# Kernel tuning notes

Hardware: AMD Instinct MI355X
Metric: run time of the kernel (lower is better)

The kernel has to match this reference:

```python
import jax, jax.numpy as jnp
import numpy as np

EPS = 1e-5

def layer_norm(x, w, b):
    mu = jnp.mean(x, axis=-1, keepdims=True)
    var = jnp.mean(jnp.square(x - mu), axis=-1, keepdims=True)
    return (x - mu) * jax.lax.rsqrt(var + EPS) * w + b

def setup_inputs() -> dict:
    key = jax.random.key(0)
    ks = jax.random.split(key, 8)
    B, T, C = 8, 512, 768
    s = 1.0 / np.sqrt(C)
    s4 = 1.0 / np.sqrt(4 * C)
    return {
        "x": jax.random.normal(ks[0], (B, T, C), dtype=jnp.float32),
        "ln1_w": jnp.ones((C,), jnp.float32),
        "ln1_b": jnp.zeros((C,), jnp.float32),
        "Wr": jax.random.normal(ks[1], (C, C), dtype=jnp.float32) * s,
        "Wk": jax.random.normal(ks[2], (C, C), dtype=jnp.float32) * s,
        "Wv": jax.random.normal(ks[3], (C, C), dtype=jnp.float32) * s,
        "time_mix_w": jnp.ones((C,), jnp.float32),  # torch init: torch.ones(n_embd)
        "Wrouter": jax.random.normal(ks[4], (C, C), dtype=jnp.float32) * s,
        "ln2_w": jnp.ones((C,), jnp.float32),
        "ln2_b": jnp.zeros((C,), jnp.float32),
        "Wck": jax.random.normal(ks[5], (4 * C, C), dtype=jnp.float32) * s,
        "Wcv": jax.random.normal(ks[6], (C, 4 * C), dtype=jnp.float32) * s4,
    }

def reference(x, ln1_w, ln1_b, Wr, Wk, Wv, time_mix_w, Wrouter, ln2_w, ln2_b, Wck, Wcv):
    B, T, C = x.shape
    xx = layer_norm(x, ln1_w, ln1_b)
    r = xx @ Wr.T
    k = xx @ Wk.T
    v = xx @ Wv.T
    w = -jnp.exp(time_mix_w)                        # (C,) negative per-channel decay rate
    idx = jnp.arange(T)
    diff = jnp.clip(idx[:, None] - idx[None, :], 0).astype(x.dtype)  # (T,T) t-j clamped at 0
    causal = jnp.tril(jnp.ones((T, T), x.dtype))
    decay = jnp.exp(w[:, None, None] * diff[None]) * causal          # (C,T,T)
    kv = k * v                                                       # (B,T,C)
    # wkv[b,t,c] = sum_j decay[c,t,j] * kv[b,j,c]
    wkv = jnp.einsum('ctj,bjc->btc', decay, kv)
    routed_wkv = wkv * jax.nn.sigmoid(xx @ Wrouter.T)
    x = x + r * routed_wkv
    xx2 = layer_norm(x, ln2_w, ln2_b)
    k_cm = jnp.square(jax.nn.relu(xx2 @ Wck.T))                      # (B,T,4C)
    return x + k_cm @ Wcv.T
```

## Files before the change

### kernel.cpp

```cpp
#include <hip/hip_runtime.h>
#include <hip/hip_bf16.h>

typedef __bf16 bf16_t;
typedef __bf16 bf16x8 __attribute__((ext_vector_type(8)));
typedef __bf16 bf16x4 __attribute__((ext_vector_type(4)));
typedef float  f32x4  __attribute__((ext_vector_type(4)));

#define LN_EPS 1e-5f


typedef __attribute__((address_space(1))) void gvoid_t;
typedef __attribute__((address_space(3))) void lvoid_t;
__device__ __forceinline__ void glds16(const void* g, void* l) {
    __builtin_amdgcn_global_load_lds((gvoid_t*)g, (lvoid_t*)l, 16, 0, 0);
}

__global__ __launch_bounds__(256) void k_cvt4(const float* __restrict__ s0,
                                              const float* __restrict__ s1,
                                              const float* __restrict__ s2,
                                              const float* __restrict__ s3,
                                              bf16_t* __restrict__ dst, int n4) {
    const float* s = (blockIdx.y == 0) ? s0 : (blockIdx.y == 1) ? s1 : (blockIdx.y == 2) ? s2 : s3;
    bf16_t* d = dst + (size_t)blockIdx.y * ((size_t)n4 * 4);
    int i = blockIdx.x * 256 + threadIdx.x;
    if (i < n4) {
        float4 v = ((const float4*)s)[i];
        bf16x4 o;
        o.x = (bf16_t)v.x; o.y = (bf16_t)v.y; o.z = (bf16_t)v.z; o.w = (bf16_t)v.w;
        ((bf16x4*)d)[i] = o;
    }
}

__global__ __launch_bounds__(256) void k_cvt2(const float* __restrict__ s0,
                                              const float* __restrict__ s1,
                                              bf16_t* __restrict__ dst, int n4) {
    const float* s = (blockIdx.y == 0) ? s0 : s1;
    bf16_t* d = dst + (size_t)blockIdx.y * ((size_t)n4 * 4);
    int i = blockIdx.x * 256 + threadIdx.x;
    if (i < n4) {
        float4 v = ((const float4*)s)[i];
        bf16x4 o;
        o.x = (bf16_t)v.x; o.y = (bf16_t)v.y; o.z = (bf16_t)v.z; o.w = (bf16_t)v.w;
        ((bf16x4*)d)[i] = o;
    }
}

__global__ __launch_bounds__(256) void k_ln(const float* __restrict__ x,
                                            const float* __restrict__ w,
                                            const float* __restrict__ b,
                                            bf16_t* __restrict__ out, int C) {
    int row = blockIdx.x;
    const float* xr = x + (long)row * C;
    int tid = threadIdx.x;
    float s = 0.f, s2 = 0.f;
    for (int i = tid; i < C; i += 256) { float v = xr[i]; s += v; s2 += v * v; }
    for (int m = 32; m; m >>= 1) { s += __shfl_xor(s, m, 64); s2 += __shfl_xor(s2, m, 64); }
    __shared__ float red[8];
    int wv = tid >> 6;
    if ((tid & 63) == 0) { red[wv] = s; red[4 + wv] = s2; }
    __syncthreads();
    float ts  = red[0] + red[1] + red[2] + red[3];
    float ts2 = red[4] + red[5] + red[6] + red[7];
    float mu  = ts / C;
    float var = ts2 / C - mu * mu;
    float rstd = rsqrtf(var + LN_EPS);
    bf16_t* orow = out + (long)row * C;
    for (int i = tid; i < C; i += 256)
        orow[i] = (bf16_t)((xr[i] - mu) * rstd * w[i] + b[i]);
}

template <int EPI>
__global__ __launch_bounds__(256) void k_gemm_bt(const bf16_t* __restrict__ A,
                                                 const bf16_t* __restrict__ Bw,
                                                 void* __restrict__ Cout,
                                                 int N, int Ktot, int nbn, int nks) {
    constexpr int TBUF = 128 * 32;
    __shared__ __align__(16) bf16_t As[3][128][32];
    __shared__ __align__(16) bf16_t Bs[3][128][32];
    const int tid  = threadIdx.x;
    const int lane = tid & 63, wid = tid >> 6;
    const int wm = (wid >> 1) * 64, wn = (wid & 1) * 64;

    int nwg = gridDim.x;
    int cpx = nwg >> 3;
    int bid = blockIdx.x;
    int swz = (bid & 7) * cpx + (bid >> 3);
    int per_m = nbn * nks;
    int bm  = swz / per_m;
    int rem = swz % per_m;
    int ks  = rem / nbn;
    int bn  = rem % nbn;

    const int fr = lane & 15;
    const int swcol = ((lane >> 4) ^ (fr & 3)) * 8;

    f32x4 acc[4][4];
#pragma unroll
    for (int i = 0; i < 4; i++)
#pragma unroll
        for (int j = 0; j < 4; j++) acc[i][j] = (f32x4){0.f, 0.f, 0.f, 0.f};

    const int srow = wid * 16 + (lane >> 2);
    const int scol = ((lane & 3) ^ ((lane >> 2) & 3)) * 8;
    const bf16_t* Ag = A  + (size_t)(bm * 128 + srow) * Ktot + (size_t)ks * 768 + scol;
    const bf16_t* Bg = Bw + (size_t)(bn * 128 + srow) * Ktot + (size_t)ks * 768 + scol;
    const size_t rowK64 = (size_t)64 * Ktot;
    bf16_t* lA = &As[0][wid * 16][0];
    bf16_t* lB = &Bs[0][wid * 16][0];

#define STAGE(buf, kt)                                              \
    do {                                                            \
        glds16(Ag + (kt),          lA + (buf) * TBUF);              \
        glds16(Ag + (kt) + rowK64, lA + (buf) * TBUF + 64 * 32);    \
        glds16(Bg + (kt),          lB + (buf) * TBUF);              \
        glds16(Bg + (kt) + rowK64, lB + (buf) * TBUF + 64 * 32);    \
    } while (0)

#define COMPUTE(buf)                                                                         \
    do {                                                                                     \
        bf16x8 af[4], bfr[4];                                                                \
        _Pragma("unroll")                                                                    \
        for (int mi = 0; mi < 4; mi++) af[mi] = *(const bf16x8*)&As[buf][wm + mi * 16 + fr][swcol]; \
        _Pragma("unroll")                                                                    \
        for (int ni = 0; ni < 4; ni++) bfr[ni] = *(const bf16x8*)&Bs[buf][wn + ni * 16 + fr][swcol]; \
        _Pragma("unroll")                                                                    \
        for (int mi = 0; mi < 4; mi++)                                                       \
            _Pragma("unroll")                                                                \
            for (int ni = 0; ni < 4; ni++)                                                   \
                acc[mi][ni] = __builtin_amdgcn_mfma_f32_16x16x32_bf16(af[mi], bfr[ni], acc[mi][ni], 0, 0, 0); \
    } while (0)

    STAGE(0, 0);
    STAGE(1, 32);
    int ba = 0, bb = 1, bc = 2;
    for (int it = 0; it < 22; ++it) {
        asm volatile("s_waitcnt vmcnt(4)" ::: "memory");
        __builtin_amdgcn_s_barrier();
        __builtin_amdgcn_sched_barrier(0);
        STAGE(bc, (it + 2) * 32);
        COMPUTE(ba);
        int t = ba; ba = bb; bb = bc; bc = t;
    }
    asm volatile("s_waitcnt vmcnt(4)" ::: "memory");
    __builtin_amdgcn_s_barrier();
    __builtin_amdgcn_sched_barrier(0);
    COMPUTE(ba);
    asm volatile("s_waitcnt vmcnt(0)" ::: "memory");
    __builtin_amdgcn_s_barrier();
    __builtin_amdgcn_sched_barrier(0);
    COMPUTE(bb);

#undef STAGE
#undef COMPUTE

    const int row0 = bm * 128 + wm, col0 = bn * 128 + wn;
#pragma unroll
    for (int mi = 0; mi < 4; mi++) {
#pragma unroll
        for (int ni = 0; ni < 4; ni++) {
            int row = row0 + mi * 16 + (lane >> 4) * 4;
            int col = col0 + ni * 16 + (lane & 15);
#pragma unroll
            for (int r = 0; r < 4; r++) {
                float val = acc[mi][ni][r];
                size_t off = (size_t)(row + r) * N + col;
                if (EPI == 0) {
                    ((bf16_t*)Cout)[off] = (bf16_t)val;
                } else if (EPI == 1) {
                    float t = fmaxf(val, 0.f);
                    ((bf16_t*)Cout)[off] = (bf16_t)(t * t);
                } else {
                    atomicAdd(&((float*)Cout)[off], val);
                }
            }
        }
    }
}

__global__ __launch_bounds__(256) void k_scan_local(const bf16_t* __restrict__ y4,
                                                    const float* __restrict__ tmw,
                                                    float* __restrict__ wkvl,
                                                    float* __restrict__ states) {
    int idx = blockIdx.x * 256 + threadIdx.x;
    int c   = idx % 768;
    int rem = idx / 768;
    int ch  = rem & 15;
    int b   = rem >> 4;
    float d = expf(-expf(tmw[c]));
    const bf16_t* base = y4 + ((size_t)(b * 512 + ch * 32)) * 3072 + c;
    float*        wout = wkvl + ((size_t)(b * 512 + ch * 32)) * 768 + c;
    float s = 0.f;
#pragma unroll 4
    for (int i = 0; i < 32; i++) {
        float kk = (float)base[(size_t)i * 3072 + 768];
        float vv = (float)base[(size_t)i * 3072 + 1536];
        s = s * d + kk * vv;
        wout[(size_t)i * 768] = s;
    }
    states[idx] = s;
}

__global__ __launch_bounds__(256) void k_scan_carry(const float* __restrict__ states,
                                                    const float* __restrict__ tmw,
                                                    float* __restrict__ carries) {
    int idx = blockIdx.x * 256 + threadIdx.x;
    int c = idx % 768, b = idx / 768;
    float dL = expf(-expf(tmw[c]) * 32.f);
    float s = 0.f;
    for (int ch = 0; ch < 16; ch++) {
        size_t o = ((size_t)(b * 16 + ch)) * 768 + c;
        carries[o] = s;
        s = s * dL + states[o];
    }
}

__global__ __launch_bounds__(256) void k_mix_ln(const bf16_t* __restrict__ y4,
                                                const float* __restrict__ wkvl,
                                                const float* __restrict__ carries,
                                                const float* __restrict__ tmw,
                                                const float* __restrict__ x,
                                                const float* __restrict__ w2,
                                                const float* __restrict__ b2,
                                                float* __restrict__ out,
                                                bf16_t* __restrict__ xx2) {
    int bt = blockIdx.x;
    int t = bt & 511, b = bt >> 9;
    int tid = threadIdx.x;
    const bf16_t* yrow = y4 + (size_t)bt * 3072;
    const float*  wl   = wkvl + (size_t)bt * 768;
    const float*  cr   = carries + ((size_t)(b * 16) + (t >> 5)) * 768;
    const float*  xr   = x + (size_t)bt * 768;
    float tn = (float)((t & 31) + 1);

    float vals[3];
    float s = 0.f, s2 = 0.f;
#pragma unroll
    for (int j = 0; j < 3; j++) {
        int c = tid + j * 256;
        float rr = (float)yrow[c];
        float gg = (float)yrow[c + 2304];
        float wk = wl[c] + cr[c] * expf(-expf(tmw[c]) * tn);
        float sig = 1.f / (1.f + expf(-gg));
        float o = fmaf(rr, wk * sig, xr[c]);
        vals[j] = o; s += o; s2 += o * o;
    }
    for (int m = 32; m; m >>= 1) { s += __shfl_xor(s, m, 64); s2 += __shfl_xor(s2, m, 64); }
    __shared__ float red[8];
    int wv = tid >> 6;
    if ((tid & 63) == 0) { red[wv] = s; red[4 + wv] = s2; }
    __syncthreads();
    float ts  = red[0] + red[1] + red[2] + red[3];
    float ts2 = red[4] + red[5] + red[6] + red[7];
    float mu  = ts * (1.f / 768.f);
    float var = ts2 * (1.f / 768.f) - mu * mu;
    float rstd = rsqrtf(var + LN_EPS);
    float* orow = out + (size_t)bt * 768;
    bf16_t* xo = xx2 + (size_t)bt * 768;
#pragma unroll
    for (int j = 0; j < 3; j++) {
        int c = tid + j * 256;
        orow[c] = vals[j];
        xo[c] = (bf16_t)((vals[j] - mu) * rstd * w2[c] + b2[c]);
    }
}

extern "C" void kernel_launch(void* const* d_in, const int* in_sizes, int n_in,
                              void* d_out, int out_size, void* d_ws, size_t ws_size,
                              hipStream_t stream) {
    const float* x    = (const float*)d_in[0];
    const float* ln1w = (const float*)d_in[1];
    const float* ln1b = (const float*)d_in[2];
    const float* Wr   = (const float*)d_in[3];
    const float* Wk   = (const float*)d_in[4];
    const float* Wv   = (const float*)d_in[5];
    const float* tmw  = (const float*)d_in[6];
    const float* Wrt  = (const float*)d_in[7];
    const float* ln2w = (const float*)d_in[8];
    const float* ln2b = (const float*)d_in[9];
    const float* Wck  = (const float*)d_in[10];
    const float* Wcv  = (const float*)d_in[11];
    float* out = (float*)d_out;
    char* ws = (char*)d_ws;

    bf16_t* xx     = (bf16_t*)(ws + 0);
    bf16_t* wcat   = (bf16_t*)(ws + 6291456);
    bf16_t* wckb   = (bf16_t*)(ws + 11010048);
    bf16_t* wcvb   = (bf16_t*)(ws + 15728640);
    bf16_t* y4     = (bf16_t*)(ws + 20447232);
    bf16_t* kcm    = (bf16_t*)(ws + 20447232);
    float*  wkvl   = (float*)(ws + 70778880);
    float*  states = (float*)(ws + 83361792);
    float*  carr   = (float*)(ws + 83755008);

    const int n768 = 768 * 768 / 4;
    const int nbig = 3072 * 768 / 4;
    k_cvt4<<<dim3(576, 4), dim3(256), 0, stream>>>(Wr, Wk, Wv, Wrt, wcat, n768);
    k_cvt2<<<dim3(2304, 2), dim3(256), 0, stream>>>(Wck, Wcv, wckb, nbig);

    k_ln<<<dim3(4096), dim3(256), 0, stream>>>(x, ln1w, ln1b, xx, 768);

    k_gemm_bt<0><<<dim3(768), dim3(256), 0, stream>>>(xx, wcat, (void*)y4, 3072, 768, 24, 1);

    k_scan_local<<<dim3(384), dim3(256), 0, stream>>>(y4, tmw, wkvl, states);
    k_scan_carry<<<dim3(24), dim3(256), 0, stream>>>(states, tmw, carr);
    k_mix_ln<<<dim3(4096), dim3(256), 0, stream>>>(y4, wkvl, carr, tmw, x, ln2w, ln2b, out, xx);

    k_gemm_bt<1><<<dim3(768), dim3(256), 0, stream>>>(xx, wckb, (void*)kcm, 3072, 768, 24, 1);

    k_gemm_bt<3><<<dim3(768), dim3(256), 0, stream>>>(kcm, wcvb, (void*)out, 768, 3072, 6, 4);
}
```

Measured before the change: 163.5 us.

## Enlarge GEMM tiles to 256x256 with 512 threads and 4-stage LDS ring

```diff
diff --git a/kernel.cpp b/kernel.cpp
--- a/kernel.cpp
+++ b/kernel.cpp
@@ -70,21 +70,19 @@
 }
 
 template <int EPI>
-__global__ __launch_bounds__(256) void k_gemm_bt(const bf16_t* __restrict__ A,
-                                                 const bf16_t* __restrict__ Bw,
-                                                 void* __restrict__ Cout,
-                                                 int N, int Ktot, int nbn, int nks) {
-    constexpr int TBUF = 128 * 32;
-    __shared__ __align__(16) bf16_t As[3][128][32];
-    __shared__ __align__(16) bf16_t Bs[3][128][32];
+__global__ __launch_bounds__(512, 2) void k_gemm_bt(const bf16_t* __restrict__ A,
+                                                    const bf16_t* __restrict__ Bw,
+                                                    void* __restrict__ Cout,
+                                                    int N, int Ktot, int nbn, int nks) {
+    constexpr int TBUF = 256 * 32;
+    __shared__ __align__(16) bf16_t As[4][256][32];
+    __shared__ __align__(16) bf16_t Bs[4][256][32];
     const int tid  = threadIdx.x;
     const int lane = tid & 63, wid = tid >> 6;
-    const int wm = (wid >> 1) * 64, wn = (wid & 1) * 64;
-
-    int nwg = gridDim.x;
-    int cpx = nwg >> 3;
+    const int wm = (wid >> 2) * 128, wn = (wid & 3) * 64;
+
     int bid = blockIdx.x;
-    int swz = (bid & 7) * cpx + (bid >> 3);
+    int swz = (bid & 7) * 24 + (bid >> 3);
     int per_m = nbn * nks;
     int bm  = swz / per_m;
     int rem = swz % per_m;
@@ -92,70 +90,74 @@
     int bn  = rem % nbn;
 
     const int fr = lane & 15;
-    const int swcol = ((lane >> 4) ^ (fr & 3)) * 8;
-
-    f32x4 acc[4][4];
-#pragma unroll
-    for (int i = 0; i < 4; i++)
+    const int swcol = (((lane >> 4) ^ (lane >> 2)) & 3) * 8;
+
+    f32x4 acc[8][4];
+#pragma unroll
+    for (int i = 0; i < 8; i++)
 #pragma unroll
         for (int j = 0; j < 4; j++) acc[i][j] = (f32x4){0.f, 0.f, 0.f, 0.f};
 
-    const int srow = wid * 16 + (lane >> 2);
-    const int scol = ((lane & 3) ^ ((lane >> 2) & 3)) * 8;
-    const bf16_t* Ag = A  + (size_t)(bm * 128 + srow) * Ktot + (size_t)ks * 768 + scol;
-    const bf16_t* Bg = Bw + (size_t)(bn * 128 + srow) * Ktot + (size_t)ks * 768 + scol;
-    const size_t rowK64 = (size_t)64 * Ktot;
-    bf16_t* lA = &As[0][wid * 16][0];
-    bf16_t* lB = &Bs[0][wid * 16][0];
-
-#define STAGE(buf, kt)                                              \
-    do {                                                            \
-        glds16(Ag + (kt),          lA + (buf) * TBUF);              \
-        glds16(Ag + (kt) + rowK64, lA + (buf) * TBUF + 64 * 32);    \
-        glds16(Bg + (kt),          lB + (buf) * TBUF);              \
-        glds16(Bg + (kt) + rowK64, lB + (buf) * TBUF + 64 * 32);    \
+    const int srow = wid * 32 + (lane >> 2);
+    const int scol = (((lane & 3) ^ (lane >> 4)) & 3) * 8;
+    const bf16_t* Ag = A  + (size_t)(bm * 256 + srow) * Ktot + (size_t)ks * 768 + scol;
+    const bf16_t* Bg = Bw + (size_t)(bn * 256 + srow) * Ktot + (size_t)ks * 768 + scol;
+    const size_t Kt16 = (size_t)16 * Ktot;
+    bf16_t* lA = &As[0][wid * 32][0];
+    bf16_t* lB = &Bs[0][wid * 32][0];
+
+#define STAGE(buf, kt)                                            \
+    do {                                                          \
+        const bf16_t* a0 = Ag + (size_t)(kt) * 32;                \
+        const bf16_t* b0 = Bg + (size_t)(kt) * 32;                \
+        glds16(a0,        lA + (buf) * TBUF);                     \
+        glds16(a0 + Kt16, lA + (buf) * TBUF + 16 * 32);           \
+        glds16(b0,        lB + (buf) * TBUF);                     \
+        glds16(b0 + Kt16, lB + (buf) * TBUF + 16 * 32);           \
     } while (0)
 
 #define COMPUTE(buf)                                                                         \
     do {                                                                                     \
-        bf16x8 af[4], bfr[4];                                                                \
+        const bf16_t* pA = &As[0][0][0] + (buf) * TBUF + (wm + fr) * 32 + swcol;             \
+        const bf16_t* pB = &Bs[0][0][0] + (buf) * TBUF + (wn + fr) * 32 + swcol;             \
+        bf16x8 af[8], bfr[4];                                                                \
         _Pragma("unroll")                                                                    \
-        for (int mi = 0; mi < 4; mi++) af[mi] = *(const bf16x8*)&As[buf][wm + mi * 16 + fr][swcol]; \
+        for (int mi = 0; mi < 8; mi++) af[mi] = *(const bf16x8*)(pA + mi * 512);             \
         _Pragma("unroll")                                                                    \
-        for (int ni = 0; ni < 4; ni++) bfr[ni] = *(const bf16x8*)&Bs[buf][wn + ni * 16 + fr][swcol]; \
+        for (int ni = 0; ni < 4; ni++) bfr[ni] = *(const bf16x8*)(pB + ni * 512);            \
+        __builtin_amdgcn_s_setprio(1);                                                       \
         _Pragma("unroll")                                                                    \
-        for (int mi = 0; mi < 4; mi++)                                                       \
+        for (int mi = 0; mi < 8; mi++)                                                       \
             _Pragma("unroll")                                                                \
             for (int ni = 0; ni < 4; ni++)                                                   \
                 acc[mi][ni] = __builtin_amdgcn_mfma_f32_16x16x32_bf16(af[mi], bfr[ni], acc[mi][ni], 0, 0, 0); \
+        __builtin_amdgcn_s_setprio(0);                                                       \
     } while (0)
 
     STAGE(0, 0);
-    STAGE(1, 32);
-    int ba = 0, bb = 1, bc = 2;
-    for (int it = 0; it < 22; ++it) {
+    STAGE(1, 1);
+    for (int s = 0; s < 22; ++s) {
         asm volatile("s_waitcnt vmcnt(4)" ::: "memory");
         __builtin_amdgcn_s_barrier();
         __builtin_amdgcn_sched_barrier(0);
-        STAGE(bc, (it + 2) * 32);
-        COMPUTE(ba);
-        int t = ba; ba = bb; bb = bc; bc = t;
+        STAGE((s + 2) & 3, s + 2);
+        COMPUTE(s & 3);
     }
     asm volatile("s_waitcnt vmcnt(4)" ::: "memory");
     __builtin_amdgcn_s_barrier();
     __builtin_amdgcn_sched_barrier(0);
-    COMPUTE(ba);
+    COMPUTE(2);
     asm volatile("s_waitcnt vmcnt(0)" ::: "memory");
     __builtin_amdgcn_s_barrier();
     __builtin_amdgcn_sched_barrier(0);
-    COMPUTE(bb);
+    COMPUTE(3);
 
 #undef STAGE
 #undef COMPUTE
 
-    const int row0 = bm * 128 + wm, col0 = bn * 128 + wn;
-#pragma unroll
-    for (int mi = 0; mi < 4; mi++) {
+    const int row0 = bm * 256 + wm, col0 = bn * 256 + wn;
+#pragma unroll
+    for (int mi = 0; mi < 8; mi++) {
 #pragma unroll
         for (int ni = 0; ni < 4; ni++) {
             int row = row0 + mi * 16 + (lane >> 4) * 4;
@@ -299,13 +301,13 @@
 
     k_ln<<<dim3(4096), dim3(256), 0, stream>>>(x, ln1w, ln1b, xx, 768);
 
-    k_gemm_bt<0><<<dim3(768), dim3(256), 0, stream>>>(xx, wcat, (void*)y4, 3072, 768, 24, 1);
+    k_gemm_bt<0><<<dim3(192), dim3(512), 0, stream>>>(xx, wcat, (void*)y4, 3072, 768, 12, 1);
 
     k_scan_local<<<dim3(384), dim3(256), 0, stream>>>(y4, tmw, wkvl, states);
     k_scan_carry<<<dim3(24), dim3(256), 0, stream>>>(states, tmw, carr);
     k_mix_ln<<<dim3(4096), dim3(256), 0, stream>>>(y4, wkvl, carr, tmw, x, ln2w, ln2b, out, xx);
 
-    k_gemm_bt<1><<<dim3(768), dim3(256), 0, stream>>>(xx, wckb, (void*)kcm, 3072, 768, 24, 1);
-
-    k_gemm_bt<3><<<dim3(768), dim3(256), 0, stream>>>(kcm, wcvb, (void*)out, 768, 3072, 6, 4);
-}
+    k_gemm_bt<1><<<dim3(192), dim3(512), 0, stream>>>(xx, wckb, (void*)kcm, 3072, 768, 12, 1);
+
+    k_gemm_bt<3><<<dim3(192), dim3(512), 0, stream>>>(kcm, wcvb, (void*)out, 768, 3072, 3, 4);
+}
```

After: 182.0 us. +11.3%, slower.
